# Kernel optimization log

Measured on AMD Instinct MI355X. Metric: run time of the kernel, lower is better.

The kernel has to match this reference:

```python
import jax, jax.numpy as jnp
import numpy as np

S, B, D_MODEL, H = 2048, 2, 1024, 16
DH = D_MODEL // H
SCALE = 1.0 / np.sqrt(DH)
NEG_INF = jnp.float32(-1e30)


def setup_inputs() -> dict:
    key = jax.random.key(0)
    ks = jax.random.split(key, 12)
    std = 1.0 / np.sqrt(D_MODEL)
    inp = {
        "query": jax.random.normal(ks[0], (S, B, D_MODEL), jnp.float32),
        "key": jax.random.normal(ks[1], (S, B, D_MODEL), jnp.float32),
        "value": jax.random.normal(ks[2], (S, B, D_MODEL), jnp.float32),
        # causal mask, shape (seq_q, seq_k, 1) per prepare_mask asserts
        "mask": jnp.tril(jnp.ones((S, S), dtype=bool))[:, :, None],
        # params stored (in, out) for x @ W
        "Wq": jax.random.normal(ks[3], (D_MODEL, H * DH), jnp.float32) * std,
        "bq": jnp.zeros((H * DH,), jnp.float32),
        "Wk": jax.random.normal(ks[4], (D_MODEL, H * DH), jnp.float32) * std,
        "bk": jnp.zeros((H * DH,), jnp.float32),
        "Wv": jax.random.normal(ks[5], (D_MODEL, H * DH), jnp.float32) * std,
        "bv": jnp.zeros((H * DH,), jnp.float32),
        "Wo": jax.random.normal(ks[6], (D_MODEL, D_MODEL), jnp.float32) * std,
        "bo": jnp.zeros((D_MODEL,), jnp.float32),
    }
    return inp


def reference(query, key, value, mask, Wq, bq, Wk, bk, Wv, bv, Wo, bo):
    seq_len, batch, _ = query.shape
    # project and split heads: (S, B, H, DH)
    q = (query @ Wq + bq).reshape(seq_len, batch, H, DH)
    k = (key @ Wk + bk).reshape(key.shape[0], batch, H, DH)
    v = (value @ Wv + bv).reshape(value.shape[0], batch, H, DH)
    # scores: (seq_q, batch, heads, seq_k)
    scores = jnp.einsum("ibhd,jbhd->ibhj", q, k) * SCALE
    # mask (seq_q, seq_k, batch_or_1) -> broadcast to (seq_q, batch, 1, seq_k)
    m = jnp.transpose(mask, (0, 2, 1))[:, :, None, :]
    scores = jnp.where(m, scores, NEG_INF)
    attn = jax.nn.softmax(scores, axis=-1)  # dropout_prob=0.0 (eval)
    x = jnp.einsum("ibhj,jbhd->ibhd", attn, v)
    x = x.reshape(seq_len, batch, H * DH)
    return x @ Wo + bo
```

## Files before the change

### kernel.cpp

```cpp
#include <hip/hip_runtime.h>
#include <hip/hip_bf16.h>
#include <cstdint>

#define S_LEN 2048
#define BATCH 2
#define DM    1024
#define NH    16
#define DH    64
#define SL2E  0.18033688011112042f

typedef short s8v __attribute__((ext_vector_type(8)));
typedef float f4v __attribute__((ext_vector_type(4)));

__device__ __forceinline__ ushort f2bf(float x) {
  union { float f; uint32_t u; } v; v.f = x;
  uint32_t r = v.u + 0x7fffu + ((v.u >> 16) & 1u);
  return (ushort)(r >> 16);
}
__device__ __forceinline__ uint32_t fbits(float x) {
  union { float f; uint32_t u; } v; v.f = x; return v.u;
}
__device__ __forceinline__ uint32_t bfrnd(uint32_t u) {
  return u + 0x7fffu + ((u >> 16) & 1u);
}
__device__ __forceinline__ uint32_t packbf(uint32_t flo, uint32_t fhi) {
  return __builtin_amdgcn_perm(bfrnd(fhi), bfrnd(flo), 0x07060302u);
}

typedef __attribute__((address_space(1))) const void gas_void;
typedef __attribute__((address_space(3))) void las_void;
__device__ __forceinline__ void gld16(void* l, const void* g) {
  __builtin_amdgcn_global_load_lds((gas_void*)(uintptr_t)g,
                                   (las_void*)(uintptr_t)l, 16, 0, 0);
}

__global__ __launch_bounds__(256)
void wtrans(const float* W0, const float* W1, const float* W2, const float* W3,
            ushort* T0, ushort* T1, ushort* T2, ushort* T3) {
  const float* W; ushort* T;
  switch (blockIdx.z) {
    case 0:  W = W0; T = T0; break;
    case 1:  W = W1; T = T1; break;
    case 2:  W = W2; T = T2; break;
    default: W = W3; T = T3; break;
  }
  __shared__ ushort tile[32][33];
  const int n0 = blockIdx.x * 32, k0 = blockIdx.y * 32;
  const int tx = threadIdx.x, ty = threadIdx.y;
  #pragma unroll
  for (int r = ty; r < 32; r += 8)
    tile[r][tx] = f2bf(W[(size_t)(k0 + r) * DM + n0 + tx]);
  __syncthreads();
  #pragma unroll
  for (int r = ty; r < 32; r += 8)
    T[(size_t)(n0 + r) * DM + k0 + tx] = tile[tx][r];
}

__global__ __launch_bounds__(256)
void castx(const float* __restrict__ X0, const float* __restrict__ X1,
           const float* __restrict__ X2,
           ushort* __restrict__ O0, ushort* __restrict__ O1,
           ushort* __restrict__ O2) {
  const float* X; ushort* O;
  switch (blockIdx.y) {
    case 0:  X = X0; O = O0; break;
    case 1:  X = X1; O = O1; break;
    default: X = X2; O = O2; break;
  }
  const size_t i = ((size_t)blockIdx.x * 256 + threadIdx.x) * 4;
  const float4 v = *(const float4*)(X + i);
  ushort4 h;
  h.x = f2bf(v.x); h.y = f2bf(v.y); h.z = f2bf(v.z); h.w = f2bf(v.w);
  *(ushort4*)(O + i) = h;
}

__global__ __launch_bounds__(256)
void gemm_qkv(const ushort* __restrict__ Xq, const ushort* __restrict__ Xk,
              const ushort* __restrict__ Xv,
              const ushort* __restrict__ Wqt, const ushort* __restrict__ Wkt,
              const ushort* __restrict__ Wvt,
              const float* __restrict__ bq, const float* __restrict__ bk,
              const float* __restrict__ bv,
              ushort* __restrict__ Qh, ushort* __restrict__ Kh,
              ushort* __restrict__ Vt) {
  const int z = blockIdx.z;
  const ushort* A    = z == 0 ? Xq  : z == 1 ? Xk  : Xv;
  const ushort* Bt   = z == 0 ? Wqt : z == 1 ? Wkt : Wvt;
  const float*  bias = z == 0 ? bq  : z == 1 ? bk  : bv;

  __shared__ __align__(16) ushort lds[20480];
  ushort* ldsA = lds;
  ushort* ldsB = lds + 8192;

  const int tid = threadIdx.x, lane = tid & 63, w = tid >> 6;
  const int wr = w >> 1, wc = w & 1;
  const int lrow = lane & 15, quad = lane >> 4;
  const int m0 = blockIdx.x * 128, n0 = blockIdx.y * 128;

  const int srow = lane >> 3;
  const int scol = ((lane & 7) ^ srow) * 8;

  const ushort* gA[4]; ushort* lA[4];
  const ushort* gB[4]; ushort* lB[4];
  #pragma unroll
  for (int t = 0; t < 4; t++) {
    const int c = 4 * w + t;
    gA[t] = A  + (size_t)(m0 + c * 8 + srow) * DM + scol;
    lA[t] = &ldsA[c * 512];
    gB[t] = Bt + (size_t)(n0 + c * 8 + srow) * DM + scol;
    lB[t] = &ldsB[c * 512];
  }

  const int f8 = lrow & 7;
  const ushort *pa[2][4], *pb[2][4];
  #pragma unroll
  for (int kk = 0; kk < 2; kk++)
    #pragma unroll
    for (int i = 0; i < 4; i++) {
      pa[kk][i] = &ldsA[(wr * 64 + i * 16 + lrow) * 64 + (((kk * 4 + quad) ^ f8) * 8)];
      pb[kk][i] = &ldsB[(wc * 64 + i * 16 + lrow) * 64 + (((kk * 4 + quad) ^ f8) * 8)];
    }

  f4v acc[4][4];
  #pragma unroll
  for (int i = 0; i < 4; i++)
    #pragma unroll
    for (int j = 0; j < 4; j++)
      acc[i][j] = f4v{0.f, 0.f, 0.f, 0.f};

  for (int k0 = 0; k0 < DM; k0 += 64) {
    __syncthreads();
    #pragma unroll
    for (int t = 0; t < 4; t++) { gld16(lA[t], gA[t] + k0); gld16(lB[t], gB[t] + k0); }
    __syncthreads();
    #pragma unroll
    for (int kk = 0; kk < 2; kk++) {
      s8v af[4], bf[4];
      #pragma unroll
      for (int i = 0; i < 4; i++) af[i] = *(const s8v*)pa[kk][i];
      #pragma unroll
      for (int j = 0; j < 4; j++) bf[j] = *(const s8v*)pb[kk][j];
      #pragma unroll
      for (int i = 0; i < 4; i++)
        #pragma unroll
        for (int j = 0; j < 4; j++)
          acc[i][j] = __builtin_amdgcn_mfma_f32_16x16x32_bf16(af[i], bf[j], acc[i][j], 0, 0, 0);
    }
  }

  if (z <= 1) {
    ushort* O = (z == 0) ? Qh : Kh;
    #pragma unroll
    for (int i = 0; i < 4; i++)
      #pragma unroll
      for (int j = 0; j < 4; j++) {
        const int n = n0 + wc * 64 + j * 16 + lrow;
        const float bval = bias[n];
        const int mb = m0 + wr * 64 + i * 16 + quad * 4;
        #pragma unroll
        for (int r = 0; r < 4; r++) {
          const int m = mb + r;
          const int s = m >> 1, b = m & 1;
          const int h = n >> 6, d = n & 63;
          O[((size_t)(b * NH + h) * S_LEN + s) * DH + d] = f2bf(acc[i][j][r] + bval);
        }
      }
  } else {
    __syncthreads();
    ushort* tw = lds + w * 5120;
    #pragma unroll
    for (int i = 0; i < 4; i++)
      #pragma unroll
      for (int j = 0; j < 4; j++) {
        const int n_l = j * 16 + lrow;
        const float bval = bias[n0 + wc * 64 + n_l];
        const int sbase = i * 8 + quad * 2;
        const uint32_t p0 = packbf(fbits(acc[i][j][0] + bval), fbits(acc[i][j][2] + bval));
        const uint32_t p1 = packbf(fbits(acc[i][j][1] + bval), fbits(acc[i][j][3] + bval));
        *(uint32_t*)&tw[n_l * 40 + sbase]        = p0;
        *(uint32_t*)&tw[2560 + n_l * 40 + sbase] = p1;
      }
    const int s0 = (m0 >> 1) + wr * 32;
    #pragma unroll
    for (int b = 0; b < 2; b++)
      #pragma unroll
      for (int p = 0; p < 4; p++) {
        const int d_l = p * 16 + (lane >> 2);
        const int c   = lane & 3;
        const s8v v = *(const s8v*)&tw[b * 2560 + d_l * 40 + c * 8];
        const int n = n0 + wc * 64 + d_l;
        const int h = n >> 6, d = n & 63;
        *(s8v*)&Vt[((size_t)(b * NH + h) * DH + d) * S_LEN + s0 + c * 8] = v;
      }
  }
}

__global__ __launch_bounds__(256)
void attn(const ushort* __restrict__ Qh, const ushort* __restrict__ Kh,
          const ushort* __restrict__ Vt, ushort* __restrict__ X,
          float* __restrict__ Opart, float* __restrict__ lpart) {
  __shared__ __align__(16) ushort Klds[2 * 64 * 64];
  __shared__ __align__(16) ushort Vlds[2 * 64 * 64];
  __shared__ __align__(16) ushort Plds[4 * 32 * 72];

  const int tid = threadIdx.x, lane = tid & 63, w = tid >> 6;
  const int lrow = lane & 15, quad = lane >> 4;
  const int bh = blockIdx.x;
  const int slot = blockIdx.y;
  int qt, jlo, jhi, part;
  if (slot < 8) { qt = slot; jlo = 0; jhi = 2 * qt + 2; part = -1; }
  else {
    const int s2 = slot - 8;
    qt = 8 + (s2 >> 1);
    const int half = s2 & 1;
    jlo = half * (qt + 1);
    jhi = jlo + (qt + 1);
    part = s2;
  }
  const int iw = qt * 128 + w * 32;

  const int srow = lane >> 3;
  const int scol = ((lane & 7) ^ srow) * 8;
  const ushort* gK0 = Kh + ((size_t)bh * S_LEN + 2 * w * 8 + srow) * DH + scol;
  const ushort* gK1 = gK0 + 8 * DH;
  const ushort* gV0 = Vt + ((size_t)bh * DH + 2 * w * 8 + srow) * S_LEN + scol;
  const ushort* gV1 = gV0 + 8 * S_LEN;
  ushort* lK0 = &Klds[2 * w * 512]; ushort* lK1 = lK0 + 512;
  ushort* lV0 = &Vlds[2 * w * 512]; ushort* lV1 = lV0 + 512;

  s8v aq[2][2];
  #pragma unroll
  for (int is = 0; is < 2; is++)
    #pragma unroll
    for (int kk = 0; kk < 2; kk++)
      aq[is][kk] = *(const s8v*)(Qh + ((size_t)bh * S_LEN + iw + is * 16 + lrow) * DH +
                                 kk * 32 + quad * 8);

  const int f8 = lrow & 7;
  const ushort* pk[4][2]; const ushort* pv[4][2]; const ushort* pp[2][2];
  #pragma unroll
  for (int s4 = 0; s4 < 4; s4++)
    #pragma unroll
    for (int kk = 0; kk < 2; kk++) {
      pk[s4][kk] = &Klds[(s4 * 16 + lrow) * 64 + (((kk * 4 + quad) ^ f8) * 8)];
      pv[s4][kk] = &Vlds[(s4 * 16 + lrow) * 64 + (((kk * 4 + quad) ^ f8) * 8)];
    }
  #pragma unroll
  for (int is = 0; is < 2; is++)
    #pragma unroll
    for (int kk = 0; kk < 2; kk++)
      pp[is][kk] = &Plds[(w * 32 + is * 16 + lrow) * 72 + kk * 32 + quad * 8];
  ushort* pw = &Plds[w * 32 * 72];

  f4v o[2][4];
  float ls[2][4];
  #pragma unroll
  for (int is = 0; is < 2; is++) {
    #pragma unroll
    for (int d4 = 0; d4 < 4; d4++) o[is][d4] = f4v{0.f, 0.f, 0.f, 0.f};
    #pragma unroll
    for (int r = 0; r < 4; r++) ls[is][r] = 0.f;
  }

  {
    const int b0 = (jlo & 1) * 4096;
    const size_t j0 = (size_t)jlo * 64;
    gld16(lK0 + b0, gK0 + j0 * DH);
    gld16(lK1 + b0, gK1 + j0 * DH);
    gld16(lV0 + b0, gV0 + j0);
    gld16(lV1 + b0, gV1 + j0);
  }

  for (int jt = jlo; jt < jhi; jt++) {
    const int j0 = jt * 64;
    __syncthreads();
    const int cur = (jt & 1) * 4096;
    if (jt + 1 < jhi) {
      const int nxt = ((jt + 1) & 1) * 4096;
      const size_t jn = (size_t)(jt + 1) * 64;
      gld16(lK0 + nxt, gK0 + jn * DH);
      gld16(lK1 + nxt, gK1 + jn * DH);
      gld16(lV0 + nxt, gV0 + jn);
      gld16(lV1 + nxt, gV1 + jn);
    }
    if (j0 > iw + 31) continue;

    f4v sc[2][4];
    #pragma unroll
    for (int is = 0; is < 2; is++)
      #pragma unroll
      for (int s4 = 0; s4 < 4; s4++) sc[is][s4] = f4v{0.f, 0.f, 0.f, 0.f};
    #pragma unroll
    for (int s4 = 0; s4 < 4; s4++) {
      const s8v b0 = *(const s8v*)(pk[s4][0] + cur);
      const s8v b1 = *(const s8v*)(pk[s4][1] + cur);
      sc[0][s4] = __builtin_amdgcn_mfma_f32_16x16x32_bf16(aq[0][0], b0, sc[0][s4], 0, 0, 0);
      sc[1][s4] = __builtin_amdgcn_mfma_f32_16x16x32_bf16(aq[1][0], b0, sc[1][s4], 0, 0, 0);
      sc[0][s4] = __builtin_amdgcn_mfma_f32_16x16x32_bf16(aq[0][1], b1, sc[0][s4], 0, 0, 0);
      sc[1][s4] = __builtin_amdgcn_mfma_f32_16x16x32_bf16(aq[1][1], b1, sc[1][s4], 0, 0, 0);
    }

    const bool needmask = (j0 + 63) > iw;
    #pragma unroll
    for (int is = 0; is < 2; is++)
      #pragma unroll
      for (int s4 = 0; s4 < 4; s4++) {
        const int jg = j0 + s4 * 16 + lrow;
        #pragma unroll
        for (int r = 0; r < 4; r++) {
          float e = exp2f(sc[is][s4][r] * SL2E);
          if (needmask) {
            const int ig = iw + is * 16 + quad * 4 + r;
            e = (jg > ig) ? 0.f : e;
          }
          ls[is][r] += e;
          pw[(is * 16 + quad * 4 + r) * 72 + s4 * 16 + lrow] = f2bf(e);
        }
      }

    s8v ap[2][2];
    #pragma unroll
    for (int is = 0; is < 2; is++)
      #pragma unroll
      for (int kk = 0; kk < 2; kk++) ap[is][kk] = *(const s8v*)pp[is][kk];

    #pragma unroll
    for (int d4 = 0; d4 < 4; d4++) {
      const s8v v0 = *(const s8v*)(pv[d4][0] + cur);
      const s8v v1 = *(const s8v*)(pv[d4][1] + cur);
      o[0][d4] = __builtin_amdgcn_mfma_f32_16x16x32_bf16(ap[0][0], v0, o[0][d4], 0, 0, 0);
      o[1][d4] = __builtin_amdgcn_mfma_f32_16x16x32_bf16(ap[1][0], v0, o[1][d4], 0, 0, 0);
      o[0][d4] = __builtin_amdgcn_mfma_f32_16x16x32_bf16(ap[0][1], v1, o[0][d4], 0, 0, 0);
      o[1][d4] = __builtin_amdgcn_mfma_f32_16x16x32_bf16(ap[1][1], v1, o[1][d4], 0, 0, 0);
    }
  }

  #pragma unroll
  for (int msk = 1; msk < 16; msk <<= 1)
    #pragma unroll
    for (int is = 0; is < 2; is++)
      #pragma unroll
      for (int r = 0; r < 4; r++)
        ls[is][r] += __shfl_xor(ls[is][r], msk, 64);

  if (part < 0) {
    const int bb = bh >> 4, h = bh & 15;
    #pragma unroll
    for (int is = 0; is < 2; is++)
      #pragma unroll
      for (int r = 0; r < 4; r++) {
        const float inv = 1.0f / ls[is][r];
        const int ig = iw + is * 16 + quad * 4 + r;
        #pragma unroll
        for (int d4 = 0; d4 < 4; d4++)
          X[((size_t)ig * BATCH + bb) * DM + h * DH + d4 * 16 + lrow] =
              f2bf(o[is][d4][r] * inv);
      }
  } else {
    float* Op = Opart + ((size_t)(bh * 16 + part)) * 8192 + (size_t)w * 32 * 64;
    #pragma unroll
    for (int is = 0; is < 2; is++)
      #pragma unroll
      for (int r = 0; r < 4; r++) {
        const int row_l = is * 16 + quad * 4 + r;
        #pragma unroll
        for (int d4 = 0; d4 < 4; d4++)
          Op[row_l * 64 + d4 * 16 + lrow] = o[is][d4][r];
      }
    if (lrow == 0) {
      float* lp = lpart + (size_t)(bh * 16 + part) * 128 + w * 32;
      #pragma unroll
      for (int is = 0; is < 2; is++)
        #pragma unroll
        for (int r = 0; r < 4; r++)
          lp[is * 16 + quad * 4 + r] = ls[is][r];
    }
  }
}

__global__ __launch_bounds__(256)
void combine(const float* __restrict__ Opart, const float* __restrict__ lpart,
             ushort* __restrict__ X) {
  const size_t gid = (size_t)blockIdx.x * 256 + threadIdx.x;
  const int dv  = gid & 15;
  const int row = (gid >> 4) & 127;
  const int bh  = (gid >> 11) & 31;
  const int qt8 = gid >> 16;
  const int pa = qt8 * 2, pb = pa + 1;
  const size_t ba = ((size_t)(bh * 16 + pa)) * 8192 + row * 64 + dv * 4;
  const size_t bb_ = ((size_t)(bh * 16 + pb)) * 8192 + row * 64 + dv * 4;
  const float4 va = *(const float4*)(Opart + ba);
  const float4 vb = *(const float4*)(Opart + bb_);
  const float l = lpart[(size_t)(bh * 16 + pa) * 128 + row] +
                  lpart[(size_t)(bh * 16 + pb) * 128 + row];
  const float inv = 1.0f / l;
  const int qpos = (qt8 + 8) * 128 + row;
  const int b = bh >> 4, h = bh & 15;
  ushort4 hv;
  hv.x = f2bf((va.x + vb.x) * inv);
  hv.y = f2bf((va.y + vb.y) * inv);
  hv.z = f2bf((va.z + vb.z) * inv);
  hv.w = f2bf((va.w + vb.w) * inv);
  *(ushort4*)&X[(((size_t)qpos * BATCH + b) * NH + h) * DH + dv * 4] = hv;
}

__global__ __launch_bounds__(256)
void gemm_out(const ushort* __restrict__ A, const ushort* __restrict__ Bt,
              const float* __restrict__ bias, float* __restrict__ C) {
  __shared__ __align__(16) ushort ldsA[128 * 64];
  __shared__ __align__(16) ushort ldsB[128 * 64];

  const int tid = threadIdx.x, lane = tid & 63, w = tid >> 6;
  const int wr = w >> 1, wc = w & 1;
  const int lrow = lane & 15, quad = lane >> 4;
  const int m0 = blockIdx.x * 128, n0 = blockIdx.y * 128;

  const int srow = lane >> 3;
  const int scol = ((lane & 7) ^ srow) * 8;

  const ushort* gA[4]; ushort* lA[4];
  const ushort* gB[4]; ushort* lB[4];
  #pragma unroll
  for (int t = 0; t < 4; t++) {
    const int c = 4 * w + t;
    gA[t] = A  + (size_t)(m0 + c * 8 + srow) * DM + scol;
    lA[t] = &ldsA[c * 512];
    gB[t] = Bt + (size_t)(n0 + c * 8 + srow) * DM + scol;
    lB[t] = &ldsB[c * 512];
  }

  const int f8 = lrow & 7;
  const ushort *pa[2][4], *pb[2][4];
  #pragma unroll
  for (int kk = 0; kk < 2; kk++)
    #pragma unroll
    for (int i = 0; i < 4; i++) {
      pa[kk][i] = &ldsA[(wr * 64 + i * 16 + lrow) * 64 + (((kk * 4 + quad) ^ f8) * 8)];
      pb[kk][i] = &ldsB[(wc * 64 + i * 16 + lrow) * 64 + (((kk * 4 + quad) ^ f8) * 8)];
    }

  f4v acc[4][4];
  #pragma unroll
  for (int i = 0; i < 4; i++)
    #pragma unroll
    for (int j = 0; j < 4; j++)
      acc[i][j] = f4v{0.f, 0.f, 0.f, 0.f};

  for (int k0 = 0; k0 < DM; k0 += 64) {
    __syncthreads();
    #pragma unroll
    for (int t = 0; t < 4; t++) { gld16(lA[t], gA[t] + k0); gld16(lB[t], gB[t] + k0); }
    __syncthreads();
    #pragma unroll
    for (int kk = 0; kk < 2; kk++) {
      s8v af[4], bf[4];
      #pragma unroll
      for (int i = 0; i < 4; i++) af[i] = *(const s8v*)pa[kk][i];
      #pragma unroll
      for (int j = 0; j < 4; j++) bf[j] = *(const s8v*)pb[kk][j];
      #pragma unroll
      for (int i = 0; i < 4; i++)
        #pragma unroll
        for (int j = 0; j < 4; j++)
          acc[i][j] = __builtin_amdgcn_mfma_f32_16x16x32_bf16(af[i], bf[j], acc[i][j], 0, 0, 0);
    }
  }

  #pragma unroll
  for (int i = 0; i < 4; i++)
    #pragma unroll
    for (int j = 0; j < 4; j++) {
      const int n = n0 + wc * 64 + j * 16 + lrow;
      const float bval = bias[n];
      const int mb = m0 + wr * 64 + i * 16 + quad * 4;
      #pragma unroll
      for (int r = 0; r < 4; r++)
        C[(size_t)(mb + r) * DM + n] = acc[i][j][r] + bval;
    }
}

extern "C" void kernel_launch(void* const* d_in, const int* in_sizes, int n_in,
                              void* d_out, int out_size, void* d_ws, size_t ws_size,
                              hipStream_t stream) {
  const float* query = (const float*)d_in[0];
  const float* key_  = (const float*)d_in[1];
  const float* value = (const float*)d_in[2];
  const float* Wq = (const float*)d_in[4];
  const float* bq = (const float*)d_in[5];
  const float* Wk = (const float*)d_in[6];
  const float* bk = (const float*)d_in[7];
  const float* Wv = (const float*)d_in[8];
  const float* bv = (const float*)d_in[9];
  const float* Wo = (const float*)d_in[10];
  const float* bo = (const float*)d_in[11];

  ushort* Wqt = (ushort*)d_ws;
  ushort* Wkt = Wqt + (size_t)1024 * 1024;
  ushort* Wvt = Wkt + (size_t)1024 * 1024;
  ushort* Wot = Wvt + (size_t)1024 * 1024;
  ushort* Xbq = Wot + (size_t)1024 * 1024;
  ushort* Xbk = Xbq + (size_t)4 * 1024 * 1024;
  ushort* Xbv = Xbk + (size_t)4 * 1024 * 1024;
  ushort* Qh  = Xbv + (size_t)4 * 1024 * 1024;
  ushort* Kh  = Qh  + (size_t)4 * 1024 * 1024;
  ushort* Vt  = Kh  + (size_t)4 * 1024 * 1024;
  float*  Opart = (float*)Xbk;
  float*  lpart = (float*)(Vt + (size_t)4 * 1024 * 1024);
  ushort* Xa  = Xbq;

  wtrans<<<dim3(32, 32, 4), dim3(32, 8), 0, stream>>>(Wq, Wk, Wv, Wo,
                                                      Wqt, Wkt, Wvt, Wot);
  castx<<<dim3(4096, 3), 256, 0, stream>>>(query, key_, value, Xbq, Xbk, Xbv);
  gemm_qkv<<<dim3(32, 8, 3), 256, 0, stream>>>(Xbq, Xbk, Xbv,
                                               Wqt, Wkt, Wvt, bq, bk, bv,
                                               Qh, Kh, Vt);
  attn<<<dim3(32, 24), 256, 0, stream>>>(Qh, Kh, Vt, Xa, Opart, lpart);
  combine<<<2048, 256, 0, stream>>>(Opart, lpart, Xa);
  gemm_out<<<dim3(32, 8), 256, 0, stream>>>(Xa, Wot, bo, (float*)d_out);
}
```

Before: 262.0 us.

## Double-buffer GEMM LDS loads, fuse prep kernels, transpose attention score layout

Merges the weight transpose and input cast into one prep launch. Both GEMMs now double-buffer their LDS tiles, so the next K slice is fetched while the current one is computed, and one of the two barriers per step goes away. The attention kernel swaps the MFMA operand order so each lane holds four consecutive keys of one query row. That lets P be written as packed uint2 stores and shrinks the row-sum to one scalar per lane, reduced with two shuffles. The cost is twice the LDS in the GEMMs (64KB per block), which may lower occupancy, and wasted idle blocks in the prep grid.

```diff
diff --git a/kernel.cpp b/kernel.cpp
--- a/kernel.cpp
+++ b/kernel.cpp
@@ -35,43 +35,34 @@
 }
 
 __global__ __launch_bounds__(256)
-void wtrans(const float* W0, const float* W1, const float* W2, const float* W3,
-            ushort* T0, ushort* T1, ushort* T2, ushort* T3) {
-  const float* W; ushort* T;
-  switch (blockIdx.z) {
-    case 0:  W = W0; T = T0; break;
-    case 1:  W = W1; T = T1; break;
-    case 2:  W = W2; T = T2; break;
-    default: W = W3; T = T3; break;
-  }
-  __shared__ ushort tile[32][33];
-  const int n0 = blockIdx.x * 32, k0 = blockIdx.y * 32;
-  const int tx = threadIdx.x, ty = threadIdx.y;
-  #pragma unroll
-  for (int r = ty; r < 32; r += 8)
-    tile[r][tx] = f2bf(W[(size_t)(k0 + r) * DM + n0 + tx]);
-  __syncthreads();
-  #pragma unroll
-  for (int r = ty; r < 32; r += 8)
-    T[(size_t)(n0 + r) * DM + k0 + tx] = tile[tx][r];
-}
-
-__global__ __launch_bounds__(256)
-void castx(const float* __restrict__ X0, const float* __restrict__ X1,
-           const float* __restrict__ X2,
-           ushort* __restrict__ O0, ushort* __restrict__ O1,
-           ushort* __restrict__ O2) {
-  const float* X; ushort* O;
-  switch (blockIdx.y) {
-    case 0:  X = X0; O = O0; break;
-    case 1:  X = X1; O = O1; break;
-    default: X = X2; O = O2; break;
-  }
-  const size_t i = ((size_t)blockIdx.x * 256 + threadIdx.x) * 4;
-  const float4 v = *(const float4*)(X + i);
-  ushort4 h;
-  h.x = f2bf(v.x); h.y = f2bf(v.y); h.z = f2bf(v.z); h.w = f2bf(v.w);
-  *(ushort4*)(O + i) = h;
+void prep(const float* W0, const float* W1, const float* W2, const float* W3,
+          ushort* T0, ushort* T1, ushort* T2, ushort* T3,
+          const float* X0, const float* X1, const float* X2,
+          ushort* O0, ushort* O1, ushort* O2) {
+  const int z = blockIdx.z;
+  if (z < 4) {
+    if (blockIdx.x >= 1024) return;
+    const float* W = z == 0 ? W0 : z == 1 ? W1 : z == 2 ? W2 : W3;
+    ushort*      T = z == 0 ? T0 : z == 1 ? T1 : z == 2 ? T2 : T3;
+    __shared__ ushort tile[32][33];
+    const int n0 = (blockIdx.x & 31) * 32, k0 = (blockIdx.x >> 5) * 32;
+    const int tx = threadIdx.x & 31, ty = threadIdx.x >> 5;
+    #pragma unroll
+    for (int r = ty; r < 32; r += 8)
+      tile[r][tx] = f2bf(W[(size_t)(k0 + r) * DM + n0 + tx]);
+    __syncthreads();
+    #pragma unroll
+    for (int r = ty; r < 32; r += 8)
+      T[(size_t)(n0 + r) * DM + k0 + tx] = tile[tx][r];
+  } else {
+    const float* X = z == 4 ? X0 : z == 5 ? X1 : X2;
+    ushort*      O = z == 4 ? O0 : z == 5 ? O1 : O2;
+    const size_t i = ((size_t)blockIdx.x * 256 + threadIdx.x) * 4;
+    const float4 v = *(const float4*)(X + i);
+    ushort4 h;
+    h.x = f2bf(v.x); h.y = f2bf(v.y); h.z = f2bf(v.z); h.w = f2bf(v.w);
+    *(ushort4*)(O + i) = h;
+  }
 }
 
 __global__ __launch_bounds__(256)
@@ -88,9 +79,7 @@
   const ushort* Bt   = z == 0 ? Wqt : z == 1 ? Wkt : Wvt;
   const float*  bias = z == 0 ? bq  : z == 1 ? bk  : bv;
 
-  __shared__ __align__(16) ushort lds[20480];
-  ushort* ldsA = lds;
-  ushort* ldsB = lds + 8192;
+  __shared__ __align__(16) ushort lds[2][16384];
 
   const int tid = threadIdx.x, lane = tid & 63, w = tid >> 6;
   const int wr = w >> 1, wc = w & 1;
@@ -100,25 +89,25 @@
   const int srow = lane >> 3;
   const int scol = ((lane & 7) ^ srow) * 8;
 
-  const ushort* gA[4]; ushort* lA[4];
-  const ushort* gB[4]; ushort* lB[4];
+  const ushort* gA[4]; const ushort* gB[4];
+  int oA[4], oB[4];
   #pragma unroll
   for (int t = 0; t < 4; t++) {
     const int c = 4 * w + t;
     gA[t] = A  + (size_t)(m0 + c * 8 + srow) * DM + scol;
-    lA[t] = &ldsA[c * 512];
+    oA[t] = c * 512;
     gB[t] = Bt + (size_t)(n0 + c * 8 + srow) * DM + scol;
-    lB[t] = &ldsB[c * 512];
+    oB[t] = 8192 + c * 512;
   }
 
   const int f8 = lrow & 7;
-  const ushort *pa[2][4], *pb[2][4];
+  int pa[2][4], pb[2][4];
   #pragma unroll
   for (int kk = 0; kk < 2; kk++)
     #pragma unroll
     for (int i = 0; i < 4; i++) {
-      pa[kk][i] = &ldsA[(wr * 64 + i * 16 + lrow) * 64 + (((kk * 4 + quad) ^ f8) * 8)];
-      pb[kk][i] = &ldsB[(wc * 64 + i * 16 + lrow) * 64 + (((kk * 4 + quad) ^ f8) * 8)];
+      pa[kk][i] = (wr * 64 + i * 16 + lrow) * 64 + (((kk * 4 + quad) ^ f8) * 8);
+      pb[kk][i] = 8192 + (wc * 64 + i * 16 + lrow) * 64 + (((kk * 4 + quad) ^ f8) * 8);
     }
 
   f4v acc[4][4];
@@ -128,18 +117,31 @@
     for (int j = 0; j < 4; j++)
       acc[i][j] = f4v{0.f, 0.f, 0.f, 0.f};
 
-  for (int k0 = 0; k0 < DM; k0 += 64) {
+  #pragma unroll
+  for (int t = 0; t < 4; t++) {
+    gld16(&lds[0][oA[t]], gA[t]);
+    gld16(&lds[0][oB[t]], gB[t]);
+  }
+
+  for (int ks = 0; ks < 16; ks++) {
     __syncthreads();
-    #pragma unroll
-    for (int t = 0; t < 4; t++) { gld16(lA[t], gA[t] + k0); gld16(lB[t], gB[t] + k0); }
-    __syncthreads();
+    const ushort* buf = lds[ks & 1];
+    if (ks < 15) {
+      ushort* nb = lds[(ks + 1) & 1];
+      const int ko = (ks + 1) * 64;
+      #pragma unroll
+      for (int t = 0; t < 4; t++) {
+        gld16(nb + oA[t], gA[t] + ko);
+        gld16(nb + oB[t], gB[t] + ko);
+      }
+    }
     #pragma unroll
     for (int kk = 0; kk < 2; kk++) {
       s8v af[4], bf[4];
       #pragma unroll
-      for (int i = 0; i < 4; i++) af[i] = *(const s8v*)pa[kk][i];
-      #pragma unroll
-      for (int j = 0; j < 4; j++) bf[j] = *(const s8v*)pb[kk][j];
+      for (int i = 0; i < 4; i++) af[i] = *(const s8v*)(buf + pa[kk][i]);
+      #pragma unroll
+      for (int j = 0; j < 4; j++) bf[j] = *(const s8v*)(buf + pb[kk][j]);
       #pragma unroll
       for (int i = 0; i < 4; i++)
         #pragma unroll
@@ -167,7 +169,7 @@
       }
   } else {
     __syncthreads();
-    ushort* tw = lds + w * 5120;
+    ushort* tw = &lds[0][0] + w * 5120;
     #pragma unroll
     for (int i = 0; i < 4; i++)
       #pragma unroll
@@ -201,7 +203,7 @@
           float* __restrict__ Opart, float* __restrict__ lpart) {
   __shared__ __align__(16) ushort Klds[2 * 64 * 64];
   __shared__ __align__(16) ushort Vlds[2 * 64 * 64];
-  __shared__ __align__(16) ushort Plds[4 * 32 * 72];
+  __shared__ __align__(16) ushort Plds[4][32 * 72];
 
   const int tid = threadIdx.x, lane = tid & 63, w = tid >> 6;
   const int lrow = lane & 15, quad = lane >> 4;
@@ -237,7 +239,7 @@
                                  kk * 32 + quad * 8);
 
   const int f8 = lrow & 7;
-  const ushort* pk[4][2]; const ushort* pv[4][2]; const ushort* pp[2][2];
+  const ushort* pk[4][2]; const ushort* pv[4][2];
   #pragma unroll
   for (int s4 = 0; s4 < 4; s4++)
     #pragma unroll
@@ -245,22 +247,14 @@
       pk[s4][kk] = &Klds[(s4 * 16 + lrow) * 64 + (((kk * 4 + quad) ^ f8) * 8)];
       pv[s4][kk] = &Vlds[(s4 * 16 + lrow) * 64 + (((kk * 4 + quad) ^ f8) * 8)];
     }
+  ushort* pwr = &Plds[w][lrow * 72];
+
+  f4v o[2][4];
+  float ls[2] = {0.f, 0.f};
   #pragma unroll
   for (int is = 0; is < 2; is++)
     #pragma unroll
-    for (int kk = 0; kk < 2; kk++)
-      pp[is][kk] = &Plds[(w * 32 + is * 16 + lrow) * 72 + kk * 32 + quad * 8];
-  ushort* pw = &Plds[w * 32 * 72];
-
-  f4v o[2][4];
-  float ls[2][4];
-  #pragma unroll
-  for (int is = 0; is < 2; is++) {
-    #pragma unroll
     for (int d4 = 0; d4 < 4; d4++) o[is][d4] = f4v{0.f, 0.f, 0.f, 0.f};
-    #pragma unroll
-    for (int r = 0; r < 4; r++) ls[is][r] = 0.f;
-  }
 
   {
     const int b0 = (jlo & 1) * 4096;
@@ -292,38 +286,45 @@
       for (int s4 = 0; s4 < 4; s4++) sc[is][s4] = f4v{0.f, 0.f, 0.f, 0.f};
     #pragma unroll
     for (int s4 = 0; s4 < 4; s4++) {
-      const s8v b0 = *(const s8v*)(pk[s4][0] + cur);
-      const s8v b1 = *(const s8v*)(pk[s4][1] + cur);
-      sc[0][s4] = __builtin_amdgcn_mfma_f32_16x16x32_bf16(aq[0][0], b0, sc[0][s4], 0, 0, 0);
-      sc[1][s4] = __builtin_amdgcn_mfma_f32_16x16x32_bf16(aq[1][0], b0, sc[1][s4], 0, 0, 0);
-      sc[0][s4] = __builtin_amdgcn_mfma_f32_16x16x32_bf16(aq[0][1], b1, sc[0][s4], 0, 0, 0);
-      sc[1][s4] = __builtin_amdgcn_mfma_f32_16x16x32_bf16(aq[1][1], b1, sc[1][s4], 0, 0, 0);
+      const s8v k0f = *(const s8v*)(pk[s4][0] + cur);
+      const s8v k1f = *(const s8v*)(pk[s4][1] + cur);
+      sc[0][s4] = __builtin_amdgcn_mfma_f32_16x16x32_bf16(k0f, aq[0][0], sc[0][s4], 0, 0, 0);
+      sc[1][s4] = __builtin_amdgcn_mfma_f32_16x16x32_bf16(k0f, aq[1][0], sc[1][s4], 0, 0, 0);
+      sc[0][s4] = __builtin_amdgcn_mfma_f32_16x16x32_bf16(k1f, aq[0][1], sc[0][s4], 0, 0, 0);
+      sc[1][s4] = __builtin_amdgcn_mfma_f32_16x16x32_bf16(k1f, aq[1][1], sc[1][s4], 0, 0, 0);
     }
 
     const bool needmask = (j0 + 63) > iw;
     #pragma unroll
+    for (int is = 0; is < 2; is++) {
+      const int ig = iw + is * 16 + lrow;
+      #pragma unroll
+      for (int s4 = 0; s4 < 4; s4++) {
+        float e0 = exp2f(sc[is][s4][0] * SL2E);
+        float e1 = exp2f(sc[is][s4][1] * SL2E);
+        float e2 = exp2f(sc[is][s4][2] * SL2E);
+        float e3 = exp2f(sc[is][s4][3] * SL2E);
+        if (needmask) {
+          const int jb = j0 + s4 * 16 + quad * 4;
+          e0 = (jb + 0 > ig) ? 0.f : e0;
+          e1 = (jb + 1 > ig) ? 0.f : e1;
+          e2 = (jb + 2 > ig) ? 0.f : e2;
+          e3 = (jb + 3 > ig) ? 0.f : e3;
+        }
+        ls[is] += (e0 + e1) + (e2 + e3);
+        uint2 pk2;
+        pk2.x = packbf(fbits(e0), fbits(e1));
+        pk2.y = packbf(fbits(e2), fbits(e3));
+        *(uint2*)&pwr[is * 16 * 72 + s4 * 16 + quad * 4] = pk2;
+      }
+    }
+
+    s8v ap[2][2];
+    #pragma unroll
     for (int is = 0; is < 2; is++)
       #pragma unroll
-      for (int s4 = 0; s4 < 4; s4++) {
-        const int jg = j0 + s4 * 16 + lrow;
-        #pragma unroll
-        for (int r = 0; r < 4; r++) {
-          float e = exp2f(sc[is][s4][r] * SL2E);
-          if (needmask) {
-            const int ig = iw + is * 16 + quad * 4 + r;
-            e = (jg > ig) ? 0.f : e;
-          }
-          ls[is][r] += e;
-          pw[(is * 16 + quad * 4 + r) * 72 + s4 * 16 + lrow] = f2bf(e);
-        }
-      }
-
-    s8v ap[2][2];
-    #pragma unroll
-    for (int is = 0; is < 2; is++)
-      #pragma unroll
-      for (int kk = 0; kk < 2; kk++) ap[is][kk] = *(const s8v*)pp[is][kk];
-
+      for (int kt = 0; kt < 2; kt++)
+        ap[is][kt] = *(const s8v*)&pwr[is * 16 * 72 + kt * 32 + quad * 8];
     #pragma unroll
     for (int d4 = 0; d4 < 4; d4++) {
       const s8v v0 = *(const s8v*)(pv[d4][0] + cur);
@@ -336,12 +337,10 @@
   }
 
   #pragma unroll
-  for (int msk = 1; msk < 16; msk <<= 1)
-    #pragma unroll
-    for (int is = 0; is < 2; is++)
-      #pragma unroll
-      for (int r = 0; r < 4; r++)
-        ls[is][r] += __shfl_xor(ls[is][r], msk, 64);
+  for (int is = 0; is < 2; is++) {
+    ls[is] += __shfl_xor(ls[is], 16, 64);
+    ls[is] += __shfl_xor(ls[is], 32, 64);
+  }
 
   if (part < 0) {
     const int bb = bh >> 4, h = bh & 15;
@@ -349,15 +348,16 @@
     for (int is = 0; is < 2; is++)
       #pragma unroll
       for (int r = 0; r < 4; r++) {
-        const float inv = 1.0f / ls[is][r];
-        const int ig = iw + is * 16 + quad * 4 + r;
+        const float lv = __shfl(ls[is], quad * 16 + quad * 4 + r, 64);
+        const float inv = 1.0f / lv;
+        const int sg = iw + is * 16 + quad * 4 + r;
         #pragma unroll
         for (int d4 = 0; d4 < 4; d4++)
-          X[((size_t)ig * BATCH + bb) * DM + h * DH + d4 * 16 + lrow] =
+          X[((size_t)sg * BATCH + bb) * DM + h * DH + d4 * 16 + lrow] =
               f2bf(o[is][d4][r] * inv);
       }
   } else {
-    float* Op = Opart + ((size_t)(bh * 16 + part)) * 8192 + (size_t)w * 32 * 64;
+    float* Op = Opart + ((size_t)(bh * 16 + part)) * 8192 + (size_t)w * 2048;
     #pragma unroll
     for (int is = 0; is < 2; is++)
       #pragma unroll
@@ -367,13 +367,10 @@
         for (int d4 = 0; d4 < 4; d4++)
           Op[row_l * 64 + d4 * 16 + lrow] = o[is][d4][r];
       }
-    if (lrow == 0) {
+    if (quad == 0) {
       float* lp = lpart + (size_t)(bh * 16 + part) * 128 + w * 32;
-      #pragma unroll
-      for (int is = 0; is < 2; is++)
-        #pragma unroll
-        for (int r = 0; r < 4; r++)
-          lp[is * 16 + quad * 4 + r] = ls[is][r];
+      lp[lrow]      = ls[0];
+      lp[16 + lrow] = ls[1];
     }
   }
 }
@@ -407,8 +404,7 @@
 __global__ __launch_bounds__(256)
 void gemm_out(const ushort* __restrict__ A, const ushort* __restrict__ Bt,
               const float* __restrict__ bias, float* __restrict__ C) {
-  __shared__ __align__(16) ushort ldsA[128 * 64];
-  __shared__ __align__(16) ushort ldsB[128 * 64];
+  __shared__ __align__(16) ushort lds[2][16384];
 
   const int tid = threadIdx.x, lane = tid & 63, w = tid >> 6;
   const int wr = w >> 1, wc = w & 1;
@@ -418,25 +414,25 @@
   const int srow = lane >> 3;
   const int scol = ((lane & 7) ^ srow) * 8;
 
-  const ushort* gA[4]; ushort* lA[4];
-  const ushort* gB[4]; ushort* lB[4];
+  const ushort* gA[4]; const ushort* gB[4];
+  int oA[4], oB[4];
   #pragma unroll
   for (int t = 0; t < 4; t++) {
     const int c = 4 * w + t;
     gA[t] = A  + (size_t)(m0 + c * 8 + srow) * DM + scol;
-    lA[t] = &ldsA[c * 512];
+    oA[t] = c * 512;
     gB[t] = Bt + (size_t)(n0 + c * 8 + srow) * DM + scol;
-    lB[t] = &ldsB[c * 512];
+    oB[t] = 8192 + c * 512;
   }
 
   const int f8 = lrow & 7;
-  const ushort *pa[2][4], *pb[2][4];
+  int pa[2][4], pb[2][4];
   #pragma unroll
   for (int kk = 0; kk < 2; kk++)
     #pragma unroll
     for (int i = 0; i < 4; i++) {
-      pa[kk][i] = &ldsA[(wr * 64 + i * 16 + lrow) * 64 + (((kk * 4 + quad) ^ f8) * 8)];
-      pb[kk][i] = &ldsB[(wc * 64 + i * 16 + lrow) * 64 + (((kk * 4 + quad) ^ f8) * 8)];
+      pa[kk][i] = (wr * 64 + i * 16 + lrow) * 64 + (((kk * 4 + quad) ^ f8) * 8);
+      pb[kk][i] = 8192 + (wc * 64 + i * 16 + lrow) * 64 + (((kk * 4 + quad) ^ f8) * 8);
     }
 
   f4v acc[4][4];
@@ -446,18 +442,31 @@
     for (int j = 0; j < 4; j++)
       acc[i][j] = f4v{0.f, 0.f, 0.f, 0.f};
 
-  for (int k0 = 0; k0 < DM; k0 += 64) {
+  #pragma unroll
+  for (int t = 0; t < 4; t++) {
+    gld16(&lds[0][oA[t]], gA[t]);
+    gld16(&lds[0][oB[t]], gB[t]);
+  }
+
+  for (int ks = 0; ks < 16; ks++) {
     __syncthreads();
-    #pragma unroll
-    for (int t = 0; t < 4; t++) { gld16(lA[t], gA[t] + k0); gld16(lB[t], gB[t] + k0); }
-    __syncthreads();
+    const ushort* buf = lds[ks & 1];
+    if (ks < 15) {
+      ushort* nb = lds[(ks + 1) & 1];
+      const int ko = (ks + 1) * 64;
+      #pragma unroll
+      for (int t = 0; t < 4; t++) {
+        gld16(nb + oA[t], gA[t] + ko);
+        gld16(nb + oB[t], gB[t] + ko);
+      }
+    }
     #pragma unroll
     for (int kk = 0; kk < 2; kk++) {
       s8v af[4], bf[4];
       #pragma unroll
-      for (int i = 0; i < 4; i++) af[i] = *(const s8v*)pa[kk][i];
-      #pragma unroll
-      for (int j = 0; j < 4; j++) bf[j] = *(const s8v*)pb[kk][j];
+      for (int i = 0; i < 4; i++) af[i] = *(const s8v*)(buf + pa[kk][i]);
+      #pragma unroll
+      for (int j = 0; j < 4; j++) bf[j] = *(const s8v*)(buf + pb[kk][j]);
       #pragma unroll
       for (int i = 0; i < 4; i++)
         #pragma unroll
@@ -508,9 +517,8 @@
   float*  lpart = (float*)(Vt + (size_t)4 * 1024 * 1024);
   ushort* Xa  = Xbq;
 
-  wtrans<<<dim3(32, 32, 4), dim3(32, 8), 0, stream>>>(Wq, Wk, Wv, Wo,
-                                                      Wqt, Wkt, Wvt, Wot);
-  castx<<<dim3(4096, 3), 256, 0, stream>>>(query, key_, value, Xbq, Xbk, Xbv);
+  prep<<<dim3(4096, 1, 7), 256, 0, stream>>>(Wq, Wk, Wv, Wo, Wqt, Wkt, Wvt, Wot,
+                                             query, key_, value, Xbq, Xbk, Xbv);
   gemm_qkv<<<dim3(32, 8, 3), 256, 0, stream>>>(Xbq, Xbk, Xbv,
                                                Wqt, Wkt, Wvt, bq, bk, bv,
                                                Qh, Kh, Vt);
```

After: 241.3 us. -7.9%, faster.
